# Kernel optimization log

Measured on AMD Instinct MI355X. Metric: run time of the kernel, lower is better.

## Reference

```python
import jax, jax.numpy as jnp
import numpy as np


def _mlp(x, Ws):
    # torch Linear(bias=False): y = x @ W.T, then leaky_relu (slope 0.01)
    for W in Ws:
        x = jax.nn.leaky_relu(x @ W.T)
    return x


def setup_inputs() -> dict:
    key = jax.random.key(0)
    ks = jax.random.split(key, 17)
    B, Cm, Hm = 128, 512, 28
    D = 2048  # NET_OUT_DIM['resnet50']
    shapes = {
        'x_mid': (B, Cm, Hm, Hm),
        'x_deep': (B, D, 7, 7),
        'w_shallow': (D, Cm),
        'ow1': (1024, D), 'ow2': (512, 1024), 'ow3': (64, 512),
        'sw1': (1024, D), 'sw2': (512, 1024), 'sw3': (64, 512),
        'tw1': (64, 128), 'tw2': (64, 64),
        'cw1': (64, 128), 'cw2': (64, 64),
        'qw1': (64, 64), 'qw2': (64, 64),
        'center': (64,), 'proto': (4, 64),
    }
    out = {}
    for k, (name, shp) in zip(ks, shapes.items()):
        scale = 1.0 if name in ('x_mid', 'x_deep', 'center', 'proto') else 0.02
        out[name] = jax.random.normal(k, shp, dtype=jnp.float32) * scale
    return out


def reference(x_mid, x_deep, w_shallow, ow1, ow2, ow3, sw1, sw2, sw3,
              tw1, tw2, cw1, cw2, qw1, qw2, center, proto):
    # shallow_conv: 1x1 conv Cm -> D
    shallow_map = jnp.einsum('bchw,oc->bohw', x_mid, w_shallow)
    # adaptive avgpool (1,1) + flatten == mean over HW
    origin = _mlp(x_deep.mean(axis=(2, 3)), [ow1, ow2, ow3])        # [B,64]
    shallow = _mlp(shallow_map.mean(axis=(2, 3)), [sw1, sw2, sw3])  # [B,64]
    texture = _mlp(jnp.concatenate([shallow, shallow - center[None]], axis=1),
                   [tw1, tw2])                                      # [B,64]
    # squared distances to each domain prototype -> [B, domain_cnt]
    sim = jnp.sum((texture[:, None, :] - proto[None, :, :]) ** 2, axis=-1)
    category = jnp.argmax(sim, axis=1)  # argmax(softmax(x)) == argmax(x)
    logp = jax.nn.log_softmax(sim, axis=1)
    ce = -jnp.mean(jnp.take_along_axis(logp, category[:, None], axis=1))
    # vectorized gather of per-sample prototype (replaces python loop)
    class_feat = jnp.concatenate([origin, origin - proto[category]], axis=1)
    class_feat = _mlp(class_feat, [cw1, cw2])
    class_svdd = jnp.sum((class_feat - center[None]) ** 2, axis=1)
    origin_svdd = jnp.sum((_mlp(origin, [qw1, qw2]) - center[None]) ** 2, axis=1)
    align = jnp.abs(origin_svdd - class_svdd)
    return jnp.stack([ce, origin_svdd.mean(), class_svdd.mean(),
                      align.mean()]).reshape(4, 1)
```

## Files before the change

kernel.cpp:

```cpp
#include <hip/hip_runtime.h>
#include <hip/hip_bf16.h>
#include <math.h>

typedef __attribute__((ext_vector_type(8))) short bf16x8;
typedef __attribute__((ext_vector_type(4))) float f32x4;

__device__ __forceinline__ float leaky(float x) { return x > 0.0f ? x : 0.01f * x; }

__device__ __forceinline__ unsigned short f2b(float f) {
    unsigned u = __builtin_bit_cast(unsigned, f);
    u += 0x7fffu + ((u >> 16) & 1u);
    return (unsigned short)(u >> 16);
}
__device__ __forceinline__ float b2f(unsigned short h) {
    unsigned u = ((unsigned)h) << 16;
    return __builtin_bit_cast(float, u);
}

__global__ __launch_bounds__(256) void means_kernel(const float* __restrict__ xm,
                                                    const float* __restrict__ xd,
                                                    unsigned short* __restrict__ xm_b,
                                                    unsigned short* __restrict__ xd_b)
{
    int blk = blockIdx.x;
    int tid = threadIdx.x;
    if (blk < 16384) {
        int lane = tid & 63;
        int wid  = tid >> 6;
        int row  = blk * 4 + wid;
        const float4* r = (const float4*)(xm + (size_t)row * 784);
        float s = 0.0f;
        for (int i = lane; i < 196; i += 64) {
            float4 v = r[i];
            s += v.x + v.y + v.z + v.w;
        }
        #pragma unroll
        for (int off = 32; off; off >>= 1) s += __shfl_xor(s, off);
        if (lane == 0) xm_b[row] = f2b(s * (1.0f / 784.0f));
    } else {
        int b2  = blk - 16384;
        int sub = tid & 15;
        int r   = tid >> 4;
        int row = b2 * 16 + r;
        const float* base = xd + (size_t)row * 49;
        float s = base[sub] + base[sub + 16] + base[sub + 32];
        if (sub == 0) s += base[48];
        #pragma unroll
        for (int off = 8; off; off >>= 1) s += __shfl_xor(s, off);
        if (sub == 0) xd_b[row] = f2b(s * (1.0f / 49.0f));
    }
}

__global__ __launch_bounds__(512) void gemm_mfma(
    const unsigned short* __restrict__ A0, const unsigned short* __restrict__ A1,
    const float* __restrict__ B0, const float* __restrict__ B1,
    float* __restrict__ P, int N, int K, int S)
{
    const int z = blockIdx.z;
    const unsigned short* A = z ? A1 : A0;
    const float*          B = z ? B1 : B0;
    const int n0 = blockIdx.x * 32;
    const int s  = blockIdx.y;
    const int Kc = K / S;
    const int k0 = s * Kc;

    const int tid = threadIdx.x;
    const int w  = tid >> 6;
    const int l  = tid & 63;
    const int lr = l & 15;
    const int lc = l >> 4;
    const int m0 = w * 16;

    const unsigned short* Ap = A + (size_t)(m0 + lr) * K + k0 + lc * 8;
    const float* Bp0 = B + (size_t)(n0 +      lr) * K + k0 + lc * 8;
    const float* Bp1 = B + (size_t)(n0 + 16 + lr) * K + k0 + lc * 8;

    f32x4 acc0 = {0.f, 0.f, 0.f, 0.f};
    f32x4 acc1 = {0.f, 0.f, 0.f, 0.f};

    for (int kt = 0; kt < Kc; kt += 32) {
        bf16x8 a = *(const bf16x8*)(Ap + kt);
        float4 u0 = *(const float4*)(Bp0 + kt);
        float4 u1 = *(const float4*)(Bp0 + kt + 4);
        float4 v0 = *(const float4*)(Bp1 + kt);
        float4 v1 = *(const float4*)(Bp1 + kt + 4);
        bf16x8 b0, b1;
        b0[0] = (short)f2b(u0.x); b0[1] = (short)f2b(u0.y);
        b0[2] = (short)f2b(u0.z); b0[3] = (short)f2b(u0.w);
        b0[4] = (short)f2b(u1.x); b0[5] = (short)f2b(u1.y);
        b0[6] = (short)f2b(u1.z); b0[7] = (short)f2b(u1.w);
        b1[0] = (short)f2b(v0.x); b1[1] = (short)f2b(v0.y);
        b1[2] = (short)f2b(v0.z); b1[3] = (short)f2b(v0.w);
        b1[4] = (short)f2b(v1.x); b1[5] = (short)f2b(v1.y);
        b1[6] = (short)f2b(v1.z); b1[7] = (short)f2b(v1.w);
        acc0 = __builtin_amdgcn_mfma_f32_16x16x32_bf16(a, b0, acc0, 0, 0, 0);
        acc1 = __builtin_amdgcn_mfma_f32_16x16x32_bf16(a, b1, acc1, 0, 0, 0);
    }

    float* Pb = P + ((size_t)(z * S + s)) * 128 * N;
    #pragma unroll
    for (int r = 0; r < 4; ++r) {
        int m = m0 + lc * 4 + r;
        Pb[(size_t)m * N + n0 + lr]      = acc0[r];
        Pb[(size_t)m * N + n0 + 16 + lr] = acc1[r];
    }
}

__global__ void reduce_b(const float* __restrict__ P,
                         unsigned short* __restrict__ out0,
                         unsigned short* __restrict__ out1,
                         int MN, int S, int paths, int do_act)
{
    int idx = blockIdx.x * blockDim.x + threadIdx.x;
    if (idx >= paths * MN) return;
    int z = idx / MN, e = idx - z * MN;
    const float* base = P + (size_t)z * S * MN;
    float s = 0.0f;
    for (int p = 0; p < S; ++p) s += base[(size_t)p * MN + e];
    if (do_act) s = leaky(s);
    unsigned short* o = z ? out1 : out0;
    o[e] = f2b(s);
}

__global__ __launch_bounds__(256) void tail_kernel(
    const float* __restrict__ PE,
    const float* __restrict__ ow3, const float* __restrict__ sw3,
    const float* __restrict__ tw1, const float* __restrict__ tw2,
    const float* __restrict__ cw1, const float* __restrict__ cw2,
    const float* __restrict__ qw1, const float* __restrict__ qw2,
    const float* __restrict__ center, const float* __restrict__ proto,
    float* __restrict__ ce_t, float* __restrict__ osv,
    float* __restrict__ csv, float* __restrict__ alv)
{
    const int b = blockIdx.x;
    const int t = threadIdx.x;
    __shared__ float o2r[512], s2r[512];
    __shared__ float red[2][64][4];
    __shared__ float o3s[64], s3s[64], t1[64], c1[64], q1[64];

    for (int e = t; e < 512; e += 256) {
        float a0 = 0.0f, a1 = 0.0f;
        #pragma unroll
        for (int p = 0; p < 8; ++p) {
            a0 += PE[(size_t)p       * 65536 + b * 512 + e];
            a1 += PE[(size_t)(8 + p) * 65536 + b * 512 + e];
        }
        o2r[e] = leaky(a0);
        s2r[e] = leaky(a1);
    }
    __syncthreads();

    {
        int o = t & 63, q = t >> 6;
        float ao = 0.0f, as_ = 0.0f;
        const float* wro = ow3 + (size_t)o * 512 + q * 128;
        const float* wrs = sw3 + (size_t)o * 512 + q * 128;
        const float* xo = o2r + q * 128;
        const float* xs = s2r + q * 128;
        for (int j = 0; j < 128; ++j) {
            ao  += wro[j] * xo[j];
            as_ += wrs[j] * xs[j];
        }
        red[0][o][q] = ao;
        red[1][o][q] = as_;
    }
    __syncthreads();
    if (t < 64) {
        o3s[t] = leaky(red[0][t][0] + red[0][t][1] + red[0][t][2] + red[0][t][3]);
        s3s[t] = leaky(red[1][t][0] + red[1][t][1] + red[1][t][2] + red[1][t][3]);
    }
    __syncthreads();

    int o = t;
    float acc;
    if (t < 64) {
        acc = 0.0f;
        for (int j = 0; j < 64; ++j) acc += tw1[o * 128 + j] * s3s[j];
        for (int j = 0; j < 64; ++j) acc += tw1[o * 128 + 64 + j] * (s3s[j] - center[j]);
        t1[o] = leaky(acc);
    }
    __syncthreads();

    float sim0 = 0, sim1 = 0, sim2 = 0, sim3 = 0;
    int cat = 0;
    float ce_val = 0;
    if (t < 64) {
        acc = 0.0f;
        for (int j = 0; j < 64; ++j) acc += tw2[o * 64 + j] * t1[j];
        float tex = leaky(acc);
        float sim[4];
        #pragma unroll
        for (int k = 0; k < 4; ++k) {
            float d = tex - proto[k * 64 + o];
            float v = d * d;
            #pragma unroll
            for (int off = 32; off; off >>= 1) v += __shfl_xor(v, off);
            sim[k] = v;
        }
        float best = sim[0];
        #pragma unroll
        for (int k = 1; k < 4; ++k) if (sim[k] > best) { best = sim[k]; cat = k; }
        float sume = 0.0f;
        #pragma unroll
        for (int k = 0; k < 4; ++k) sume += expf(sim[k] - best);
        ce_val = logf(sume);
        acc = 0.0f;
        for (int j = 0; j < 64; ++j) acc += cw1[o * 128 + j] * o3s[j];
        for (int j = 0; j < 64; ++j) acc += cw1[o * 128 + 64 + j] * (o3s[j] - proto[cat * 64 + j]);
        c1[o] = leaky(acc);
    }
    __syncthreads();
    if (t < 64) {
        acc = 0.0f;
        for (int j = 0; j < 64; ++j) acc += cw2[o * 64 + j] * c1[j];
        float cf = leaky(acc);
        float dc = cf - center[o];
        float cs = dc * dc;
        #pragma unroll
        for (int off = 32; off; off >>= 1) cs += __shfl_xor(cs, off);
        acc = 0.0f;
        for (int j = 0; j < 64; ++j) acc += qw1[o * 64 + j] * o3s[j];
        q1[o] = leaky(acc);
        c1[o] = 0.0f;
        red[0][o][0] = cs;
    }
    __syncthreads();
    if (t < 64) {
        acc = 0.0f;
        for (int j = 0; j < 64; ++j) acc += qw2[o * 64 + j] * q1[j];
        float qf = leaky(acc);
        float dq = qf - center[o];
        float os = dq * dq;
        #pragma unroll
        for (int off = 32; off; off >>= 1) os += __shfl_xor(os, off);
        if (o == 0) {
            float cs = red[0][0][0];
            ce_t[b] = ce_val;
            osv[b]  = os;
            csv[b]  = cs;
            alv[b]  = fabsf(os - cs);
        }
    }
}

__global__ __launch_bounds__(128) void finalize_kernel(
    const float* __restrict__ ce_t, const float* __restrict__ osv,
    const float* __restrict__ csv, const float* __restrict__ alv,
    float* __restrict__ out)
{
    int t = threadIdx.x;
    float v[4] = { ce_t[t], osv[t], csv[t], alv[t] };
    __shared__ float tmp[4][2];
    int lane = t & 63, w = t >> 6;
    #pragma unroll
    for (int i = 0; i < 4; ++i) {
        float x = v[i];
        #pragma unroll
        for (int off = 32; off; off >>= 1) x += __shfl_xor(x, off);
        if (lane == 0) tmp[i][w] = x;
    }
    __syncthreads();
    if (t < 4) out[t] = (tmp[t][0] + tmp[t][1]) * (1.0f / 128.0f);
}

extern "C" void kernel_launch(void* const* d_in, const int* in_sizes, int n_in,
                              void* d_out, int out_size, void* d_ws, size_t ws_size,
                              hipStream_t stream)
{
    const float* x_mid     = (const float*)d_in[0];
    const float* x_deep    = (const float*)d_in[1];
    const float* w_shallow = (const float*)d_in[2];
    const float* ow1 = (const float*)d_in[3];
    const float* ow2 = (const float*)d_in[4];
    const float* ow3 = (const float*)d_in[5];
    const float* sw1 = (const float*)d_in[6];
    const float* sw2 = (const float*)d_in[7];
    const float* sw3 = (const float*)d_in[8];
    const float* tw1 = (const float*)d_in[9];
    const float* tw2 = (const float*)d_in[10];
    const float* cw1 = (const float*)d_in[11];
    const float* cw2 = (const float*)d_in[12];
    const float* qw1 = (const float*)d_in[13];
    const float* qw2 = (const float*)d_in[14];
    const float* center = (const float*)d_in[15];
    const float* proto  = (const float*)d_in[16];
    float* out = (float*)d_out;

    char* wb = (char*)d_ws;
    unsigned short* xm_b = (unsigned short*)(wb);
    unsigned short* xd_b = (unsigned short*)(wb + (1<<20));
    unsigned short* sh_b = (unsigned short*)(wb + (2<<20));
    unsigned short* o1_b = (unsigned short*)(wb + (3<<20));
    unsigned short* s1_b = (unsigned short*)(wb + (4<<20));
    float* P_C  = (float*)(wb + (8<<20));
    float* P_D  = (float*)(wb + (16<<20));
    float* P_E  = (float*)(wb + (32<<20));
    float* ce_t = (float*)(wb + (48<<20));
    float* osv  = ce_t + 128;
    float* csv  = ce_t + 256;
    float* alv  = ce_t + 384;

    means_kernel<<<32768, 256, 0, stream>>>(x_mid, x_deep, xm_b, xd_b);

    gemm_mfma<<<dim3(64, 4, 1), 512, 0, stream>>>(
        xm_b, nullptr, w_shallow, nullptr, P_C, 2048, 512, 4);
    reduce_b<<<1024, 256, 0, stream>>>(P_C, sh_b, nullptr, 262144, 4, 1, 0);

    gemm_mfma<<<dim3(32, 8, 2), 512, 0, stream>>>(
        xd_b, sh_b, ow1, sw1, P_D, 1024, 2048, 8);
    reduce_b<<<1024, 256, 0, stream>>>(P_D, o1_b, s1_b, 131072, 8, 2, 1);

    gemm_mfma<<<dim3(16, 8, 2), 512, 0, stream>>>(
        o1_b, s1_b, ow2, sw2, P_E, 512, 1024, 8);

    tail_kernel<<<128, 256, 0, stream>>>(P_E, ow3, sw3, tw1, tw2, cw1, cw2,
                                         qw1, qw2, center, proto,
                                         ce_t, osv, csv, alv);

    finalize_kernel<<<1, 128, 0, stream>>>(ce_t, osv, csv, alv, out);
}
```

Measured before the change: 112.2 us.

## Fuse GEMM chain, reductions and tail into one cooperative persistent kernel

Replaces the three split-K GEMM launches, two reduction kernels, tail kernel and finalize kernel with a single cooperative kernel of 256 blocks separated by grid-wide syncs. Split-K partial sums, and the leaky activation where needed, are now reduced on the fly while loading the next GEMM's A operand, so the separate bf16 intermediate buffers go away. The split factors change (4 instead of 8 for layer one) to fit the fixed grid. The aim is to remove launch overhead and reduction passes, at the cost of grid-sync latency, redundant re-reads of partial sums by every N-tile block, and fewer blocks per stage.

```diff
diff --git a/kernel.cpp b/kernel.cpp
--- a/kernel.cpp
+++ b/kernel.cpp
@@ -1,6 +1,9 @@
 #include <hip/hip_runtime.h>
+#include <hip/hip_cooperative_groups.h>
 #include <hip/hip_bf16.h>
 #include <math.h>
+
+namespace cg = cooperative_groups;
 
 typedef __attribute__((ext_vector_type(8))) short bf16x8;
 typedef __attribute__((ext_vector_type(4))) float f32x4;
@@ -12,9 +15,14 @@
     u += 0x7fffu + ((u >> 16) & 1u);
     return (unsigned short)(u >> 16);
 }
-__device__ __forceinline__ float b2f(unsigned short h) {
-    unsigned u = ((unsigned)h) << 16;
-    return __builtin_bit_cast(float, u);
+
+__device__ __forceinline__ bf16x8 cvt8(float4 u0, float4 u1) {
+    bf16x8 r;
+    r[0] = (short)f2b(u0.x); r[1] = (short)f2b(u0.y);
+    r[2] = (short)f2b(u0.z); r[3] = (short)f2b(u0.w);
+    r[4] = (short)f2b(u1.x); r[5] = (short)f2b(u1.y);
+    r[6] = (short)f2b(u1.z); r[7] = (short)f2b(u1.w);
+    return r;
 }
 
 __global__ __launch_bounds__(256) void means_kernel(const float* __restrict__ xm,
@@ -51,216 +59,265 @@
     }
 }
 
-__global__ __launch_bounds__(512) void gemm_mfma(
-    const unsigned short* __restrict__ A0, const unsigned short* __restrict__ A1,
-    const float* __restrict__ B0, const float* __restrict__ B1,
-    float* __restrict__ P, int N, int K, int S)
+__global__ __launch_bounds__(512, 2) void mega_kernel(
+    char* __restrict__ ws,
+    const float* __restrict__ w_shallow,
+    const float* __restrict__ ow1, const float* __restrict__ ow2, const float* __restrict__ ow3,
+    const float* __restrict__ sw1, const float* __restrict__ sw2, const float* __restrict__ sw3,
+    const float* __restrict__ tw1, const float* __restrict__ tw2,
+    const float* __restrict__ cw1, const float* __restrict__ cw2,
+    const float* __restrict__ qw1, const float* __restrict__ qw2,
+    const float* __restrict__ center, const float* __restrict__ proto,
+    float* __restrict__ out)
 {
-    const int z = blockIdx.z;
-    const unsigned short* A = z ? A1 : A0;
-    const float*          B = z ? B1 : B0;
-    const int n0 = blockIdx.x * 32;
-    const int s  = blockIdx.y;
-    const int Kc = K / S;
-    const int k0 = s * Kc;
+    cg::grid_group grid = cg::this_grid();
+
+    const unsigned short* xm_b = (const unsigned short*)(ws);
+    const unsigned short* xd_b = (const unsigned short*)(ws + (1 << 20));
+    float* P_C  = (float*)(ws + (8 << 20));
+    float* P_D  = (float*)(ws + (16 << 20));
+    float* P_E  = (float*)(ws + (32 << 20));
+    float* ce_t = (float*)(ws + (48 << 20));
+    float* osv  = ce_t + 128;
+    float* csv  = ce_t + 256;
+    float* alv  = ce_t + 384;
 
     const int tid = threadIdx.x;
+    const int bid = blockIdx.x;
     const int w  = tid >> 6;
     const int l  = tid & 63;
     const int lr = l & 15;
     const int lc = l >> 4;
     const int m0 = w * 16;
 
-    const unsigned short* Ap = A + (size_t)(m0 + lr) * K + k0 + lc * 8;
-    const float* Bp0 = B + (size_t)(n0 +      lr) * K + k0 + lc * 8;
-    const float* Bp1 = B + (size_t)(n0 + 16 + lr) * K + k0 + lc * 8;
-
-    f32x4 acc0 = {0.f, 0.f, 0.f, 0.f};
-    f32x4 acc1 = {0.f, 0.f, 0.f, 0.f};
-
-    for (int kt = 0; kt < Kc; kt += 32) {
-        bf16x8 a = *(const bf16x8*)(Ap + kt);
-        float4 u0 = *(const float4*)(Bp0 + kt);
-        float4 u1 = *(const float4*)(Bp0 + kt + 4);
-        float4 v0 = *(const float4*)(Bp1 + kt);
-        float4 v1 = *(const float4*)(Bp1 + kt + 4);
-        bf16x8 b0, b1;
-        b0[0] = (short)f2b(u0.x); b0[1] = (short)f2b(u0.y);
-        b0[2] = (short)f2b(u0.z); b0[3] = (short)f2b(u0.w);
-        b0[4] = (short)f2b(u1.x); b0[5] = (short)f2b(u1.y);
-        b0[6] = (short)f2b(u1.z); b0[7] = (short)f2b(u1.w);
-        b1[0] = (short)f2b(v0.x); b1[1] = (short)f2b(v0.y);
-        b1[2] = (short)f2b(v0.z); b1[3] = (short)f2b(v0.w);
-        b1[4] = (short)f2b(v1.x); b1[5] = (short)f2b(v1.y);
-        b1[6] = (short)f2b(v1.z); b1[7] = (short)f2b(v1.w);
-        acc0 = __builtin_amdgcn_mfma_f32_16x16x32_bf16(a, b0, acc0, 0, 0, 0);
-        acc1 = __builtin_amdgcn_mfma_f32_16x16x32_bf16(a, b1, acc1, 0, 0, 0);
-    }
-
-    float* Pb = P + ((size_t)(z * S + s)) * 128 * N;
-    #pragma unroll
-    for (int r = 0; r < 4; ++r) {
-        int m = m0 + lc * 4 + r;
-        Pb[(size_t)m * N + n0 + lr]      = acc0[r];
-        Pb[(size_t)m * N + n0 + 16 + lr] = acc1[r];
-    }
-}
-
-__global__ void reduce_b(const float* __restrict__ P,
-                         unsigned short* __restrict__ out0,
-                         unsigned short* __restrict__ out1,
-                         int MN, int S, int paths, int do_act)
-{
-    int idx = blockIdx.x * blockDim.x + threadIdx.x;
-    if (idx >= paths * MN) return;
-    int z = idx / MN, e = idx - z * MN;
-    const float* base = P + (size_t)z * S * MN;
-    float s = 0.0f;
-    for (int p = 0; p < S; ++p) s += base[(size_t)p * MN + e];
-    if (do_act) s = leaky(s);
-    unsigned short* o = z ? out1 : out0;
-    o[e] = f2b(s);
-}
-
-__global__ __launch_bounds__(256) void tail_kernel(
-    const float* __restrict__ PE,
-    const float* __restrict__ ow3, const float* __restrict__ sw3,
-    const float* __restrict__ tw1, const float* __restrict__ tw2,
-    const float* __restrict__ cw1, const float* __restrict__ cw2,
-    const float* __restrict__ qw1, const float* __restrict__ qw2,
-    const float* __restrict__ center, const float* __restrict__ proto,
-    float* __restrict__ ce_t, float* __restrict__ osv,
-    float* __restrict__ csv, float* __restrict__ alv)
-{
-    const int b = blockIdx.x;
-    const int t = threadIdx.x;
     __shared__ float o2r[512], s2r[512];
     __shared__ float red[2][64][4];
-    __shared__ float o3s[64], s3s[64], t1[64], c1[64], q1[64];
-
-    for (int e = t; e < 512; e += 256) {
-        float a0 = 0.0f, a1 = 0.0f;
-        #pragma unroll
-        for (int p = 0; p < 8; ++p) {
-            a0 += PE[(size_t)p       * 65536 + b * 512 + e];
-            a1 += PE[(size_t)(8 + p) * 65536 + b * 512 + e];
-        }
-        o2r[e] = leaky(a0);
-        s2r[e] = leaky(a1);
-    }
-    __syncthreads();
+    __shared__ float o3s[64], s3s[64], t1s[64], c1s[64], q1s[64];
+    __shared__ float tmp[4][8];
 
     {
-        int o = t & 63, q = t >> 6;
-        float ao = 0.0f, as_ = 0.0f;
-        const float* wro = ow3 + (size_t)o * 512 + q * 128;
-        const float* wrs = sw3 + (size_t)o * 512 + q * 128;
-        const float* xo = o2r + q * 128;
-        const float* xs = s2r + q * 128;
-        for (int j = 0; j < 128; ++j) {
-            ao  += wro[j] * xo[j];
-            as_ += wrs[j] * xs[j];
-        }
-        red[0][o][q] = ao;
-        red[1][o][q] = as_;
-    }
-    __syncthreads();
-    if (t < 64) {
-        o3s[t] = leaky(red[0][t][0] + red[0][t][1] + red[0][t][2] + red[0][t][3]);
-        s3s[t] = leaky(red[1][t][0] + red[1][t][1] + red[1][t][2] + red[1][t][3]);
-    }
-    __syncthreads();
-
-    int o = t;
-    float acc;
-    if (t < 64) {
-        acc = 0.0f;
-        for (int j = 0; j < 64; ++j) acc += tw1[o * 128 + j] * s3s[j];
-        for (int j = 0; j < 64; ++j) acc += tw1[o * 128 + 64 + j] * (s3s[j] - center[j]);
-        t1[o] = leaky(acc);
-    }
-    __syncthreads();
-
-    float sim0 = 0, sim1 = 0, sim2 = 0, sim3 = 0;
-    int cat = 0;
-    float ce_val = 0;
-    if (t < 64) {
-        acc = 0.0f;
-        for (int j = 0; j < 64; ++j) acc += tw2[o * 64 + j] * t1[j];
-        float tex = leaky(acc);
-        float sim[4];
-        #pragma unroll
-        for (int k = 0; k < 4; ++k) {
-            float d = tex - proto[k * 64 + o];
-            float v = d * d;
-            #pragma unroll
-            for (int off = 32; off; off >>= 1) v += __shfl_xor(v, off);
-            sim[k] = v;
-        }
-        float best = sim[0];
-        #pragma unroll
-        for (int k = 1; k < 4; ++k) if (sim[k] > best) { best = sim[k]; cat = k; }
-        float sume = 0.0f;
-        #pragma unroll
-        for (int k = 0; k < 4; ++k) sume += expf(sim[k] - best);
-        ce_val = logf(sume);
-        acc = 0.0f;
-        for (int j = 0; j < 64; ++j) acc += cw1[o * 128 + j] * o3s[j];
-        for (int j = 0; j < 64; ++j) acc += cw1[o * 128 + 64 + j] * (o3s[j] - proto[cat * 64 + j]);
-        c1[o] = leaky(acc);
-    }
-    __syncthreads();
-    if (t < 64) {
-        acc = 0.0f;
-        for (int j = 0; j < 64; ++j) acc += cw2[o * 64 + j] * c1[j];
-        float cf = leaky(acc);
-        float dc = cf - center[o];
-        float cs = dc * dc;
-        #pragma unroll
-        for (int off = 32; off; off >>= 1) cs += __shfl_xor(cs, off);
-        acc = 0.0f;
-        for (int j = 0; j < 64; ++j) acc += qw1[o * 64 + j] * o3s[j];
-        q1[o] = leaky(acc);
-        c1[o] = 0.0f;
-        red[0][o][0] = cs;
-    }
-    __syncthreads();
-    if (t < 64) {
-        acc = 0.0f;
-        for (int j = 0; j < 64; ++j) acc += qw2[o * 64 + j] * q1[j];
-        float qf = leaky(acc);
-        float dq = qf - center[o];
-        float os = dq * dq;
-        #pragma unroll
-        for (int off = 32; off; off >>= 1) os += __shfl_xor(os, off);
-        if (o == 0) {
-            float cs = red[0][0][0];
-            ce_t[b] = ce_val;
-            osv[b]  = os;
-            csv[b]  = cs;
-            alv[b]  = fabsf(os - cs);
-        }
-    }
-}
-
-__global__ __launch_bounds__(128) void finalize_kernel(
-    const float* __restrict__ ce_t, const float* __restrict__ osv,
-    const float* __restrict__ csv, const float* __restrict__ alv,
-    float* __restrict__ out)
-{
-    int t = threadIdx.x;
-    float v[4] = { ce_t[t], osv[t], csv[t], alv[t] };
-    __shared__ float tmp[4][2];
-    int lane = t & 63, w = t >> 6;
-    #pragma unroll
-    for (int i = 0; i < 4; ++i) {
-        float x = v[i];
-        #pragma unroll
-        for (int off = 32; off; off >>= 1) x += __shfl_xor(x, off);
-        if (lane == 0) tmp[i][w] = x;
-    }
-    __syncthreads();
-    if (t < 4) out[t] = (tmp[t][0] + tmp[t][1]) * (1.0f / 128.0f);
+        const int nt = bid >> 2, s = bid & 3;
+        const int n0 = nt * 32;
+        const int K = 512, Kc = 128, k0 = s * Kc;
+        const unsigned short* Ap = xm_b + (size_t)(m0 + lr) * K + k0 + lc * 8;
+        const float* Bp0 = w_shallow + (size_t)(n0 + lr) * K + k0 + lc * 8;
+        const float* Bp1 = Bp0 + (size_t)16 * K;
+        f32x4 acc0 = {0.f,0.f,0.f,0.f}, acc1 = {0.f,0.f,0.f,0.f};
+        for (int kt = 0; kt < Kc; kt += 32) {
+            bf16x8 a  = *(const bf16x8*)(Ap + kt);
+            bf16x8 b0 = cvt8(*(const float4*)(Bp0 + kt), *(const float4*)(Bp0 + kt + 4));
+            bf16x8 b1 = cvt8(*(const float4*)(Bp1 + kt), *(const float4*)(Bp1 + kt + 4));
+            acc0 = __builtin_amdgcn_mfma_f32_16x16x32_bf16(a, b0, acc0, 0, 0, 0);
+            acc1 = __builtin_amdgcn_mfma_f32_16x16x32_bf16(a, b1, acc1, 0, 0, 0);
+        }
+        float* Pb = P_C + (size_t)s * (128 * 2048);
+        #pragma unroll
+        for (int r = 0; r < 4; ++r) {
+            int m = m0 + lc * 4 + r;
+            Pb[(size_t)m * 2048 + n0 + lr]      = acc0[r];
+            Pb[(size_t)m * 2048 + n0 + 16 + lr] = acc1[r];
+        }
+    }
+    grid.sync();
+
+    {
+        const int z  = bid >> 7;
+        const int r7 = bid & 127;
+        const int nt = r7 >> 2, s = r7 & 3;
+        const int n0 = nt * 32;
+        const int K = 2048, Kc = 512, k0 = s * Kc;
+        const float* Bsel = z ? sw1 : ow1;
+        const float* Bp0 = Bsel + (size_t)(n0 + lr) * K + k0 + lc * 8;
+        const float* Bp1 = Bp0 + (size_t)16 * K;
+        const size_t aoff0 = (size_t)(m0 + lr) * K + k0 + lc * 8;
+        f32x4 acc0 = {0.f,0.f,0.f,0.f}, acc1 = {0.f,0.f,0.f,0.f};
+        for (int kt = 0; kt < Kc; kt += 32) {
+            bf16x8 a;
+            if (z == 0) {
+                a = *(const bf16x8*)(xd_b + aoff0 + kt);
+            } else {
+                float s0[8] = {0,0,0,0,0,0,0,0};
+                #pragma unroll
+                for (int p = 0; p < 4; ++p) {
+                    const float* q = P_C + (size_t)p * (128 * 2048) + aoff0 + kt;
+                    float4 u = *(const float4*)q;
+                    float4 v = *(const float4*)(q + 4);
+                    s0[0] += u.x; s0[1] += u.y; s0[2] += u.z; s0[3] += u.w;
+                    s0[4] += v.x; s0[5] += v.y; s0[6] += v.z; s0[7] += v.w;
+                }
+                #pragma unroll
+                for (int j = 0; j < 8; ++j) a[j] = (short)f2b(s0[j]);
+            }
+            bf16x8 b0 = cvt8(*(const float4*)(Bp0 + kt), *(const float4*)(Bp0 + kt + 4));
+            bf16x8 b1 = cvt8(*(const float4*)(Bp1 + kt), *(const float4*)(Bp1 + kt + 4));
+            acc0 = __builtin_amdgcn_mfma_f32_16x16x32_bf16(a, b0, acc0, 0, 0, 0);
+            acc1 = __builtin_amdgcn_mfma_f32_16x16x32_bf16(a, b1, acc1, 0, 0, 0);
+        }
+        float* Pb = P_D + (size_t)(z * 4 + s) * (128 * 1024);
+        #pragma unroll
+        for (int r = 0; r < 4; ++r) {
+            int m = m0 + lc * 4 + r;
+            Pb[(size_t)m * 1024 + n0 + lr]      = acc0[r];
+            Pb[(size_t)m * 1024 + n0 + 16 + lr] = acc1[r];
+        }
+    }
+    grid.sync();
+
+    {
+        const int z  = bid >> 7;
+        const int r7 = bid & 127;
+        const int nt = r7 >> 3, s = r7 & 7;
+        const int n0 = nt * 32;
+        const int K = 1024, Kc = 128, k0 = s * Kc;
+        const float* Bsel = z ? sw2 : ow2;
+        const float* Bp0 = Bsel + (size_t)(n0 + lr) * K + k0 + lc * 8;
+        const float* Bp1 = Bp0 + (size_t)16 * K;
+        const float* Abase = P_D + (size_t)z * 4 * (128 * 1024);
+        const size_t aoff0 = (size_t)(m0 + lr) * K + k0 + lc * 8;
+        f32x4 acc0 = {0.f,0.f,0.f,0.f}, acc1 = {0.f,0.f,0.f,0.f};
+        for (int kt = 0; kt < Kc; kt += 32) {
+            float s0[8] = {0,0,0,0,0,0,0,0};
+            #pragma unroll
+            for (int p = 0; p < 4; ++p) {
+                const float* q = Abase + (size_t)p * (128 * 1024) + aoff0 + kt;
+                float4 u = *(const float4*)q;
+                float4 v = *(const float4*)(q + 4);
+                s0[0] += u.x; s0[1] += u.y; s0[2] += u.z; s0[3] += u.w;
+                s0[4] += v.x; s0[5] += v.y; s0[6] += v.z; s0[7] += v.w;
+            }
+            bf16x8 a;
+            #pragma unroll
+            for (int j = 0; j < 8; ++j) a[j] = (short)f2b(leaky(s0[j]));
+            bf16x8 b0 = cvt8(*(const float4*)(Bp0 + kt), *(const float4*)(Bp0 + kt + 4));
+            bf16x8 b1 = cvt8(*(const float4*)(Bp1 + kt), *(const float4*)(Bp1 + kt + 4));
+            acc0 = __builtin_amdgcn_mfma_f32_16x16x32_bf16(a, b0, acc0, 0, 0, 0);
+            acc1 = __builtin_amdgcn_mfma_f32_16x16x32_bf16(a, b1, acc1, 0, 0, 0);
+        }
+        float* Pb = P_E + (size_t)(z * 8 + s) * (128 * 512);
+        #pragma unroll
+        for (int r = 0; r < 4; ++r) {
+            int m = m0 + lc * 4 + r;
+            Pb[(size_t)m * 512 + n0 + lr]      = acc0[r];
+            Pb[(size_t)m * 512 + n0 + 16 + lr] = acc1[r];
+        }
+    }
+    grid.sync();
+
+    if (bid < 128) {
+        const int b = bid;
+        {
+            int e = tid;
+            float a0 = 0.f, a1 = 0.f;
+            #pragma unroll
+            for (int p = 0; p < 8; ++p) {
+                a0 += P_E[(size_t)p       * 65536 + b * 512 + e];
+                a1 += P_E[(size_t)(8 + p) * 65536 + b * 512 + e];
+            }
+            o2r[e] = leaky(a0);
+            s2r[e] = leaky(a1);
+        }
+        __syncthreads();
+        {
+            int p = tid >> 8, o = (tid >> 2) & 63, q = tid & 3;
+            const float* wr = (p ? sw3 : ow3) + (size_t)o * 512 + q * 128;
+            const float* xr = (p ? s2r : o2r) + q * 128;
+            float acc = 0.f;
+            for (int j = 0; j < 128; ++j) acc += wr[j] * xr[j];
+            red[p][o][q] = acc;
+        }
+        __syncthreads();
+        if (tid < 128) {
+            int p = tid >> 6, o = tid & 63;
+            float v = leaky(red[p][o][0] + red[p][o][1] + red[p][o][2] + red[p][o][3]);
+            if (p) s3s[o] = v; else o3s[o] = v;
+        }
+        __syncthreads();
+
+        float ce_val = 0.f;
+        int o = tid;
+        if (tid < 64) {
+            float acc = 0.f;
+            for (int j = 0; j < 64; ++j) acc += tw1[o * 128 + j] * s3s[j];
+            for (int j = 0; j < 64; ++j) acc += tw1[o * 128 + 64 + j] * (s3s[j] - center[j]);
+            t1s[o] = leaky(acc);
+        }
+        __syncthreads();
+        if (tid < 64) {
+            float acc = 0.f;
+            for (int j = 0; j < 64; ++j) acc += tw2[o * 64 + j] * t1s[j];
+            float tex = leaky(acc);
+            float sim[4];
+            #pragma unroll
+            for (int k = 0; k < 4; ++k) {
+                float d = tex - proto[k * 64 + o];
+                float v = d * d;
+                #pragma unroll
+                for (int off = 32; off; off >>= 1) v += __shfl_xor(v, off);
+                sim[k] = v;
+            }
+            int cat = 0; float best = sim[0];
+            #pragma unroll
+            for (int k = 1; k < 4; ++k) if (sim[k] > best) { best = sim[k]; cat = k; }
+            float sume = 0.f;
+            #pragma unroll
+            for (int k = 0; k < 4; ++k) sume += expf(sim[k] - best);
+            ce_val = logf(sume);
+            acc = 0.f;
+            for (int j = 0; j < 64; ++j) acc += cw1[o * 128 + j] * o3s[j];
+            for (int j = 0; j < 64; ++j) acc += cw1[o * 128 + 64 + j] * (o3s[j] - proto[cat * 64 + j]);
+            c1s[o] = leaky(acc);
+            acc = 0.f;
+            for (int j = 0; j < 64; ++j) acc += qw1[o * 64 + j] * o3s[j];
+            q1s[o] = leaky(acc);
+        }
+        __syncthreads();
+        if (tid < 64) {
+            float acc = 0.f;
+            for (int j = 0; j < 64; ++j) acc += cw2[o * 64 + j] * c1s[j];
+            float cf = leaky(acc);
+            float dc = cf - center[o];
+            float cs = dc * dc;
+            #pragma unroll
+            for (int off = 32; off; off >>= 1) cs += __shfl_xor(cs, off);
+            acc = 0.f;
+            for (int j = 0; j < 64; ++j) acc += qw2[o * 64 + j] * q1s[j];
+            float qf = leaky(acc);
+            float dq = qf - center[o];
+            float os = dq * dq;
+            #pragma unroll
+            for (int off = 32; off; off >>= 1) os += __shfl_xor(os, off);
+            if (o == 0) {
+                ce_t[b] = ce_val;
+                osv[b]  = os;
+                csv[b]  = cs;
+                alv[b]  = fabsf(os - cs);
+            }
+        }
+    }
+    grid.sync();
+
+    if (bid == 0) {
+        float v0 = 0.f, v1 = 0.f, v2 = 0.f, v3 = 0.f;
+        if (tid < 128) {
+            v0 = ce_t[tid]; v1 = osv[tid]; v2 = csv[tid]; v3 = alv[tid];
+        }
+        float v[4] = { v0, v1, v2, v3 };
+        int lane = tid & 63, wv = tid >> 6;
+        #pragma unroll
+        for (int i = 0; i < 4; ++i) {
+            float x = v[i];
+            #pragma unroll
+            for (int off = 32; off; off >>= 1) x += __shfl_xor(x, off);
+            if (lane == 0) tmp[i][wv] = x;
+        }
+        __syncthreads();
+        if (tid < 4) {
+            float s = 0.f;
+            #pragma unroll
+            for (int j = 0; j < 8; ++j) s += tmp[tid][j];
+            out[tid] = s * (1.0f / 128.0f);
+        }
+    }
 }
 
 extern "C" void kernel_launch(void* const* d_in, const int* in_sizes, int n_in,
@@ -286,36 +343,21 @@
     const float* proto  = (const float*)d_in[16];
     float* out = (float*)d_out;
 
-    char* wb = (char*)d_ws;
-    unsigned short* xm_b = (unsigned short*)(wb);
-    unsigned short* xd_b = (unsigned short*)(wb + (1<<20));
-    unsigned short* sh_b = (unsigned short*)(wb + (2<<20));
-    unsigned short* o1_b = (unsigned short*)(wb + (3<<20));
-    unsigned short* s1_b = (unsigned short*)(wb + (4<<20));
-    float* P_C  = (float*)(wb + (8<<20));
-    float* P_D  = (float*)(wb + (16<<20));
-    float* P_E  = (float*)(wb + (32<<20));
-    float* ce_t = (float*)(wb + (48<<20));
-    float* osv  = ce_t + 128;
-    float* csv  = ce_t + 256;
-    float* alv  = ce_t + 384;
+    char* ws = (char*)d_ws;
+    unsigned short* xm_b = (unsigned short*)(ws);
+    unsigned short* xd_b = (unsigned short*)(ws + (1 << 20));
 
     means_kernel<<<32768, 256, 0, stream>>>(x_mid, x_deep, xm_b, xd_b);
 
-    gemm_mfma<<<dim3(64, 4, 1), 512, 0, stream>>>(
-        xm_b, nullptr, w_shallow, nullptr, P_C, 2048, 512, 4);
-    reduce_b<<<1024, 256, 0, stream>>>(P_C, sh_b, nullptr, 262144, 4, 1, 0);
-
-    gemm_mfma<<<dim3(32, 8, 2), 512, 0, stream>>>(
-        xd_b, sh_b, ow1, sw1, P_D, 1024, 2048, 8);
-    reduce_b<<<1024, 256, 0, stream>>>(P_D, o1_b, s1_b, 131072, 8, 2, 1);
-
-    gemm_mfma<<<dim3(16, 8, 2), 512, 0, stream>>>(
-        o1_b, s1_b, ow2, sw2, P_E, 512, 1024, 8);
-
-    tail_kernel<<<128, 256, 0, stream>>>(P_E, ow3, sw3, tw1, tw2, cw1, cw2,
-                                         qw1, qw2, center, proto,
-                                         ce_t, osv, csv, alv);
-
-    finalize_kernel<<<1, 128, 0, stream>>>(ce_t, osv, csv, alv, out);
-}
+    void* kargs[] = {
+        (void*)&ws, (void*)&w_shallow,
+        (void*)&ow1, (void*)&ow2, (void*)&ow3,
+        (void*)&sw1, (void*)&sw2, (void*)&sw3,
+        (void*)&tw1, (void*)&tw2,
+        (void*)&cw1, (void*)&cw2,
+        (void*)&qw1, (void*)&qw2,
+        (void*)&center, (void*)&proto, (void*)&out
+    };
+    hipLaunchCooperativeKernel((void*)mega_kernel, dim3(256), dim3(512),
+                               kargs, 0, stream);
+}
```

Result: slower. 247.4 us (+120.5%).

## Drop split-K, fuse epilogues into GEMMs, pair layers into staggered launches

Applied to the files above, without the earlier changes.

Replaces the split-K GEMMs plus separate reduction kernels with full-K GEMM blocks that apply leaky ReLU and write bf16 directly. The origin and shallow branches are staggered so that each launch runs one layer of each path. The ow3 layer moves into a GEMM, and the final mean is done with atomics into an output zeroed by the means kernel. This removes the partial-sum traffic and several launches, but leaves far fewer blocks, each with long serial K loops.

```diff
diff --git a/kernel.cpp b/kernel.cpp
--- a/kernel.cpp
+++ b/kernel.cpp
@@ -17,13 +17,24 @@
     return __builtin_bit_cast(float, u);
 }
 
+__device__ __forceinline__ bf16x8 cvt8(float4 u0, float4 u1) {
+    bf16x8 r;
+    r[0] = (short)f2b(u0.x); r[1] = (short)f2b(u0.y);
+    r[2] = (short)f2b(u0.z); r[3] = (short)f2b(u0.w);
+    r[4] = (short)f2b(u1.x); r[5] = (short)f2b(u1.y);
+    r[6] = (short)f2b(u1.z); r[7] = (short)f2b(u1.w);
+    return r;
+}
+
 __global__ __launch_bounds__(256) void means_kernel(const float* __restrict__ xm,
                                                     const float* __restrict__ xd,
                                                     unsigned short* __restrict__ xm_b,
-                                                    unsigned short* __restrict__ xd_b)
+                                                    unsigned short* __restrict__ xd_b,
+                                                    float* __restrict__ out)
 {
     int blk = blockIdx.x;
     int tid = threadIdx.x;
+    if (blk == 0 && tid < 4) out[tid] = 0.0f;
     if (blk < 16384) {
         int lane = tid & 63;
         int wid  = tid >> 6;
@@ -51,142 +62,111 @@
     }
 }
 
-__global__ __launch_bounds__(512) void gemm_mfma(
-    const unsigned short* __restrict__ A0, const unsigned short* __restrict__ A1,
-    const float* __restrict__ B0, const float* __restrict__ B1,
-    float* __restrict__ P, int N, int K, int S)
-{
-    const int z = blockIdx.z;
-    const unsigned short* A = z ? A1 : A0;
-    const float*          B = z ? B1 : B0;
-    const int n0 = blockIdx.x * 32;
-    const int s  = blockIdx.y;
-    const int Kc = K / S;
-    const int k0 = s * Kc;
-
-    const int tid = threadIdx.x;
+__device__ __forceinline__ void gemm_block(
+    const unsigned short* __restrict__ Ab, const float* __restrict__ Bw,
+    unsigned short* __restrict__ Ob, int N, int K, int n0, int act, int tid)
+{
     const int w  = tid >> 6;
     const int l  = tid & 63;
     const int lr = l & 15;
     const int lc = l >> 4;
     const int m0 = w * 16;
 
-    const unsigned short* Ap = A + (size_t)(m0 + lr) * K + k0 + lc * 8;
-    const float* Bp0 = B + (size_t)(n0 +      lr) * K + k0 + lc * 8;
-    const float* Bp1 = B + (size_t)(n0 + 16 + lr) * K + k0 + lc * 8;
-
-    f32x4 acc0 = {0.f, 0.f, 0.f, 0.f};
-    f32x4 acc1 = {0.f, 0.f, 0.f, 0.f};
-
-    for (int kt = 0; kt < Kc; kt += 32) {
-        bf16x8 a = *(const bf16x8*)(Ap + kt);
-        float4 u0 = *(const float4*)(Bp0 + kt);
-        float4 u1 = *(const float4*)(Bp0 + kt + 4);
-        float4 v0 = *(const float4*)(Bp1 + kt);
-        float4 v1 = *(const float4*)(Bp1 + kt + 4);
-        bf16x8 b0, b1;
-        b0[0] = (short)f2b(u0.x); b0[1] = (short)f2b(u0.y);
-        b0[2] = (short)f2b(u0.z); b0[3] = (short)f2b(u0.w);
-        b0[4] = (short)f2b(u1.x); b0[5] = (short)f2b(u1.y);
-        b0[6] = (short)f2b(u1.z); b0[7] = (short)f2b(u1.w);
-        b1[0] = (short)f2b(v0.x); b1[1] = (short)f2b(v0.y);
-        b1[2] = (short)f2b(v0.z); b1[3] = (short)f2b(v0.w);
-        b1[4] = (short)f2b(v1.x); b1[5] = (short)f2b(v1.y);
-        b1[6] = (short)f2b(v1.z); b1[7] = (short)f2b(v1.w);
+    const unsigned short* Ap = Ab + (size_t)(m0 + lr) * K + lc * 8;
+    const float* Bp0 = Bw + (size_t)(n0 + lr) * K + lc * 8;
+    const float* Bp1 = Bp0 + (size_t)16 * K;
+
+    f32x4 acc0 = {0.f,0.f,0.f,0.f}, acc1 = {0.f,0.f,0.f,0.f};
+    for (int kt = 0; kt < K; kt += 32) {
+        bf16x8 a  = *(const bf16x8*)(Ap + kt);
+        bf16x8 b0 = cvt8(*(const float4*)(Bp0 + kt), *(const float4*)(Bp0 + kt + 4));
+        bf16x8 b1 = cvt8(*(const float4*)(Bp1 + kt), *(const float4*)(Bp1 + kt + 4));
         acc0 = __builtin_amdgcn_mfma_f32_16x16x32_bf16(a, b0, acc0, 0, 0, 0);
         acc1 = __builtin_amdgcn_mfma_f32_16x16x32_bf16(a, b1, acc1, 0, 0, 0);
     }
-
-    float* Pb = P + ((size_t)(z * S + s)) * 128 * N;
     #pragma unroll
     for (int r = 0; r < 4; ++r) {
         int m = m0 + lc * 4 + r;
-        Pb[(size_t)m * N + n0 + lr]      = acc0[r];
-        Pb[(size_t)m * N + n0 + 16 + lr] = acc1[r];
-    }
-}
-
-__global__ void reduce_b(const float* __restrict__ P,
-                         unsigned short* __restrict__ out0,
-                         unsigned short* __restrict__ out1,
-                         int MN, int S, int paths, int do_act)
-{
-    int idx = blockIdx.x * blockDim.x + threadIdx.x;
-    if (idx >= paths * MN) return;
-    int z = idx / MN, e = idx - z * MN;
-    const float* base = P + (size_t)z * S * MN;
-    float s = 0.0f;
-    for (int p = 0; p < S; ++p) s += base[(size_t)p * MN + e];
-    if (do_act) s = leaky(s);
-    unsigned short* o = z ? out1 : out0;
-    o[e] = f2b(s);
+        float v0 = acc0[r], v1 = acc1[r];
+        if (act) { v0 = leaky(v0); v1 = leaky(v1); }
+        Ob[(size_t)m * N + n0 + lr]      = f2b(v0);
+        Ob[(size_t)m * N + n0 + 16 + lr] = f2b(v1);
+    }
+}
+
+__global__ __launch_bounds__(512) void gemm_a(
+    const unsigned short* __restrict__ xm_b, const unsigned short* __restrict__ xd_b,
+    const float* __restrict__ w_shallow, const float* __restrict__ ow1,
+    unsigned short* __restrict__ sh_b, unsigned short* __restrict__ o1_b)
+{
+    int bid = blockIdx.x, tid = threadIdx.x;
+    if (bid < 64) gemm_block(xm_b, w_shallow, sh_b, 2048, 512,  bid * 32,        0, tid);
+    else          gemm_block(xd_b, ow1,       o1_b, 1024, 2048, (bid - 64) * 32, 1, tid);
+}
+
+__global__ __launch_bounds__(512) void gemm_b(
+    const unsigned short* __restrict__ sh_b, const unsigned short* __restrict__ o1_b,
+    const float* __restrict__ sw1, const float* __restrict__ ow2,
+    unsigned short* __restrict__ s1_b, unsigned short* __restrict__ o2_b)
+{
+    int bid = blockIdx.x, tid = threadIdx.x;
+    if (bid < 32) gemm_block(sh_b, sw1, s1_b, 1024, 2048, bid * 32,        1, tid);
+    else          gemm_block(o1_b, ow2, o2_b, 512,  1024, (bid - 32) * 32, 1, tid);
+}
+
+__global__ __launch_bounds__(512) void gemm_c(
+    const unsigned short* __restrict__ s1_b, const unsigned short* __restrict__ o2_b,
+    const float* __restrict__ sw2, const float* __restrict__ ow3,
+    unsigned short* __restrict__ s2_b, unsigned short* __restrict__ o3_b)
+{
+    int bid = blockIdx.x, tid = threadIdx.x;
+    if (bid < 16) gemm_block(s1_b, sw2, s2_b, 512, 1024, bid * 32,        1, tid);
+    else          gemm_block(o2_b, ow3, o3_b, 64,  512,  (bid - 16) * 32, 1, tid);
 }
 
 __global__ __launch_bounds__(256) void tail_kernel(
-    const float* __restrict__ PE,
-    const float* __restrict__ ow3, const float* __restrict__ sw3,
+    const unsigned short* __restrict__ s2_b, const unsigned short* __restrict__ o3_b,
+    const float* __restrict__ sw3,
     const float* __restrict__ tw1, const float* __restrict__ tw2,
     const float* __restrict__ cw1, const float* __restrict__ cw2,
     const float* __restrict__ qw1, const float* __restrict__ qw2,
     const float* __restrict__ center, const float* __restrict__ proto,
-    float* __restrict__ ce_t, float* __restrict__ osv,
-    float* __restrict__ csv, float* __restrict__ alv)
+    float* __restrict__ out)
 {
     const int b = blockIdx.x;
     const int t = threadIdx.x;
-    __shared__ float o2r[512], s2r[512];
-    __shared__ float red[2][64][4];
-    __shared__ float o3s[64], s3s[64], t1[64], c1[64], q1[64];
-
-    for (int e = t; e < 512; e += 256) {
-        float a0 = 0.0f, a1 = 0.0f;
-        #pragma unroll
-        for (int p = 0; p < 8; ++p) {
-            a0 += PE[(size_t)p       * 65536 + b * 512 + e];
-            a1 += PE[(size_t)(8 + p) * 65536 + b * 512 + e];
-        }
-        o2r[e] = leaky(a0);
-        s2r[e] = leaky(a1);
-    }
+    __shared__ float s2r[512];
+    __shared__ float red[64][4];
+    __shared__ float o3s[64], s3s[64], t1s[64], c1s[64], q1s[64];
+
+    for (int e = t; e < 512; e += 256) s2r[e] = b2f(s2_b[b * 512 + e]);
+    if (t < 64) o3s[t] = b2f(o3_b[b * 64 + t]);
     __syncthreads();
 
     {
         int o = t & 63, q = t >> 6;
-        float ao = 0.0f, as_ = 0.0f;
-        const float* wro = ow3 + (size_t)o * 512 + q * 128;
-        const float* wrs = sw3 + (size_t)o * 512 + q * 128;
-        const float* xo = o2r + q * 128;
-        const float* xs = s2r + q * 128;
-        for (int j = 0; j < 128; ++j) {
-            ao  += wro[j] * xo[j];
-            as_ += wrs[j] * xs[j];
-        }
-        red[0][o][q] = ao;
-        red[1][o][q] = as_;
-    }
-    __syncthreads();
+        const float* wr = sw3 + (size_t)o * 512 + q * 128;
+        const float* xr = s2r + q * 128;
+        float acc = 0.f;
+        for (int j = 0; j < 128; ++j) acc += wr[j] * xr[j];
+        red[o][q] = acc;
+    }
+    __syncthreads();
+    if (t < 64) s3s[t] = leaky(red[t][0] + red[t][1] + red[t][2] + red[t][3]);
+    __syncthreads();
+
+    float ce_val = 0.f;
+    int o = t;
     if (t < 64) {
-        o3s[t] = leaky(red[0][t][0] + red[0][t][1] + red[0][t][2] + red[0][t][3]);
-        s3s[t] = leaky(red[1][t][0] + red[1][t][1] + red[1][t][2] + red[1][t][3]);
-    }
-    __syncthreads();
-
-    int o = t;
-    float acc;
-    if (t < 64) {
-        acc = 0.0f;
+        float acc = 0.f;
         for (int j = 0; j < 64; ++j) acc += tw1[o * 128 + j] * s3s[j];
         for (int j = 0; j < 64; ++j) acc += tw1[o * 128 + 64 + j] * (s3s[j] - center[j]);
-        t1[o] = leaky(acc);
-    }
-    __syncthreads();
-
-    float sim0 = 0, sim1 = 0, sim2 = 0, sim3 = 0;
-    int cat = 0;
-    float ce_val = 0;
+        t1s[o] = leaky(acc);
+    }
+    __syncthreads();
     if (t < 64) {
-        acc = 0.0f;
-        for (int j = 0; j < 64; ++j) acc += tw2[o * 64 + j] * t1[j];
+        float acc = 0.f;
+        for (int j = 0; j < 64; ++j) acc += tw2[o * 64 + j] * t1s[j];
         float tex = leaky(acc);
         float sim[4];
         #pragma unroll
@@ -197,70 +177,44 @@
             for (int off = 32; off; off >>= 1) v += __shfl_xor(v, off);
             sim[k] = v;
         }
-        float best = sim[0];
+        int cat = 0; float best = sim[0];
         #pragma unroll
         for (int k = 1; k < 4; ++k) if (sim[k] > best) { best = sim[k]; cat = k; }
-        float sume = 0.0f;
+        float sume = 0.f;
         #pragma unroll
         for (int k = 0; k < 4; ++k) sume += expf(sim[k] - best);
         ce_val = logf(sume);
-        acc = 0.0f;
+        acc = 0.f;
         for (int j = 0; j < 64; ++j) acc += cw1[o * 128 + j] * o3s[j];
         for (int j = 0; j < 64; ++j) acc += cw1[o * 128 + 64 + j] * (o3s[j] - proto[cat * 64 + j]);
-        c1[o] = leaky(acc);
+        c1s[o] = leaky(acc);
+        acc = 0.f;
+        for (int j = 0; j < 64; ++j) acc += qw1[o * 64 + j] * o3s[j];
+        q1s[o] = leaky(acc);
     }
     __syncthreads();
     if (t < 64) {
-        acc = 0.0f;
-        for (int j = 0; j < 64; ++j) acc += cw2[o * 64 + j] * c1[j];
+        float acc = 0.f;
+        for (int j = 0; j < 64; ++j) acc += cw2[o * 64 + j] * c1s[j];
         float cf = leaky(acc);
         float dc = cf - center[o];
         float cs = dc * dc;
         #pragma unroll
         for (int off = 32; off; off >>= 1) cs += __shfl_xor(cs, off);
-        acc = 0.0f;
-        for (int j = 0; j < 64; ++j) acc += qw1[o * 64 + j] * o3s[j];
-        q1[o] = leaky(acc);
-        c1[o] = 0.0f;
-        red[0][o][0] = cs;
-    }
-    __syncthreads();
-    if (t < 64) {
-        acc = 0.0f;
-        for (int j = 0; j < 64; ++j) acc += qw2[o * 64 + j] * q1[j];
+        acc = 0.f;
+        for (int j = 0; j < 64; ++j) acc += qw2[o * 64 + j] * q1s[j];
         float qf = leaky(acc);
         float dq = qf - center[o];
         float os = dq * dq;
         #pragma unroll
         for (int off = 32; off; off >>= 1) os += __shfl_xor(os, off);
         if (o == 0) {
-            float cs = red[0][0][0];
-            ce_t[b] = ce_val;
-            osv[b]  = os;
-            csv[b]  = cs;
-            alv[b]  = fabsf(os - cs);
+            atomicAdd(out + 0, ce_val * (1.0f / 128.0f));
+            atomicAdd(out + 1, os     * (1.0f / 128.0f));
+            atomicAdd(out + 2, cs     * (1.0f / 128.0f));
+            atomicAdd(out + 3, fabsf(os - cs) * (1.0f / 128.0f));
         }
     }
-}
-
-__global__ __launch_bounds__(128) void finalize_kernel(
-    const float* __restrict__ ce_t, const float* __restrict__ osv,
-    const float* __restrict__ csv, const float* __restrict__ alv,
-    float* __restrict__ out)
-{
-    int t = threadIdx.x;
-    float v[4] = { ce_t[t], osv[t], csv[t], alv[t] };
-    __shared__ float tmp[4][2];
-    int lane = t & 63, w = t >> 6;
-    #pragma unroll
-    for (int i = 0; i < 4; ++i) {
-        float x = v[i];
-        #pragma unroll
-        for (int off = 32; off; off >>= 1) x += __shfl_xor(x, off);
-        if (lane == 0) tmp[i][w] = x;
-    }
-    __syncthreads();
-    if (t < 4) out[t] = (tmp[t][0] + tmp[t][1]) * (1.0f / 128.0f);
 }
 
 extern "C" void kernel_launch(void* const* d_in, const int* in_sizes, int n_in,
@@ -286,36 +240,22 @@
     const float* proto  = (const float*)d_in[16];
     float* out = (float*)d_out;
 
-    char* wb = (char*)d_ws;
-    unsigned short* xm_b = (unsigned short*)(wb);
-    unsigned short* xd_b = (unsigned short*)(wb + (1<<20));
-    unsigned short* sh_b = (unsigned short*)(wb + (2<<20));
-    unsigned short* o1_b = (unsigned short*)(wb + (3<<20));
-    unsigned short* s1_b = (unsigned short*)(wb + (4<<20));
-    float* P_C  = (float*)(wb + (8<<20));
-    float* P_D  = (float*)(wb + (16<<20));
-    float* P_E  = (float*)(wb + (32<<20));
-    float* ce_t = (float*)(wb + (48<<20));
-    float* osv  = ce_t + 128;
-    float* csv  = ce_t + 256;
-    float* alv  = ce_t + 384;
-
-    means_kernel<<<32768, 256, 0, stream>>>(x_mid, x_deep, xm_b, xd_b);
-
-    gemm_mfma<<<dim3(64, 4, 1), 512, 0, stream>>>(
-        xm_b, nullptr, w_shallow, nullptr, P_C, 2048, 512, 4);
-    reduce_b<<<1024, 256, 0, stream>>>(P_C, sh_b, nullptr, 262144, 4, 1, 0);
-
-    gemm_mfma<<<dim3(32, 8, 2), 512, 0, stream>>>(
-        xd_b, sh_b, ow1, sw1, P_D, 1024, 2048, 8);
-    reduce_b<<<1024, 256, 0, stream>>>(P_D, o1_b, s1_b, 131072, 8, 2, 1);
-
-    gemm_mfma<<<dim3(16, 8, 2), 512, 0, stream>>>(
-        o1_b, s1_b, ow2, sw2, P_E, 512, 1024, 8);
-
-    tail_kernel<<<128, 256, 0, stream>>>(P_E, ow3, sw3, tw1, tw2, cw1, cw2,
-                                         qw1, qw2, center, proto,
-                                         ce_t, osv, csv, alv);
-
-    finalize_kernel<<<1, 128, 0, stream>>>(ce_t, osv, csv, alv, out);
-}
+    char* ws = (char*)d_ws;
+    unsigned short* xm_b = (unsigned short*)(ws);
+    unsigned short* xd_b = (unsigned short*)(ws + (1 << 20));
+    unsigned short* sh_b = (unsigned short*)(ws + (2 << 20));
+    unsigned short* o1_b = (unsigned short*)(ws + (3 << 20));
+    unsigned short* s1_b = (unsigned short*)(ws + (4 << 20));
+    unsigned short* o2_b = (unsigned short*)(ws + (5 << 20));
+    unsigned short* s2_b = (unsigned short*)(ws + (6 << 20));
+    unsigned short* o3_b = (unsigned short*)(ws + (7 << 20));
+
+    means_kernel<<<32768, 256, 0, stream>>>(x_mid, x_deep, xm_b, xd_b, out);
+
+    gemm_a<<<96, 512, 0, stream>>>(xm_b, xd_b, w_shallow, ow1, sh_b, o1_b);
+    gemm_b<<<48, 512, 0, stream>>>(sh_b, o1_b, sw1, ow2, s1_b, o2_b);
+    gemm_c<<<18, 512, 0, stream>>>(s1_b, o2_b, sw2, ow3, s2_b, o3_b);
+
+    tail_kernel<<<128, 256, 0, stream>>>(s2_b, o3_b, sw3, tw1, tw2, cw1, cw2,
+                                         qw1, qw2, center, proto, out);
+}
```

New measurement: 247.4 us. 120% more time.
